# Kernel tuning notes

Hardware: AMD Instinct MI355X
Metric: run time of the kernel (lower is better)

## Reference

```python
import jax, jax.numpy as jnp
import numpy as np


def setup_inputs() -> dict:
    key = jax.random.key(0)
    n_samples, n_points, dims = 16, 2048, 64
    h = jax.random.normal(key, (n_samples, n_points, dims), dtype=jnp.float32)
    return {"h": h, "K": 16}


def reference(h, K):
    """Pairwise squared distance + K nearest neighbors -> edge list.

    h : (n_samples, n_points, dims)
    Returns (knn_dist, dst, src):
      knn_dist : (n_samples, n_points, K) squared distances to the K nearest points
      dst, src : (n_samples*n_points*K,) int32 globally-offset edge endpoints
    """
    n_samples, n_points, _ = h.shape
    # d[b, i, j] = ||h[b,i]||^2 + ||h[b,j]||^2 - 2 <h[b,i], h[b,j]>
    x2s = jnp.sum(h * h, axis=-1, keepdims=True)          # (s, n, 1)
    d = x2s + jnp.swapaxes(x2s, -1, -2) - 2.0 * jnp.einsum('bnd,bmd->bnm', h, h)
    # smallest-K == top-K of negated distances (matches torch.topk largest=False order)
    neg_vals, k_indices = jax.lax.top_k(-d, K)            # (s, n, K)
    knn_dist = -neg_vals
    # edge list with per-sample node-id offsets (matches the torch flattening)
    src = jnp.broadcast_to(jnp.arange(n_points, dtype=k_indices.dtype)[None, :, None],
                           k_indices.shape)
    offset = (jnp.arange(n_samples, dtype=k_indices.dtype) * n_points)[:, None, None]
    dst = (k_indices + offset).reshape(-1)
    src = (src + offset).reshape(-1)
    return knn_dist, dst, src
```

## Files before the change

### kernel.cpp

```cpp
#include <hip/hip_runtime.h>
#include <hip/hip_fp16.h>
#include <cfloat>


typedef _Float16 half8 __attribute__((ext_vector_type(8)));
typedef _Float16 half4 __attribute__((ext_vector_type(4)));
typedef float    f32x4 __attribute__((ext_vector_type(4)));

constexpr int NS = 16, NP = 2048, ND = 64, KK = 16;
constexpr int NWV = 4;
constexpr int NT  = NWV * 64;
constexpr int RB  = 64;
constexpr int ITN = RB / 16;
constexpr int JW  = NP / NWV;
constexpr int NJT = JW / 16;
constexpr int MS  = 17;
constexpr int RCAP = 176;
constexpr int RSTR = RCAP + 1;
constexpr float MARGIN = 1.0f;

__global__ __launch_bounds__(256)
void prep_kernel(const float* __restrict__ h, float* __restrict__ x2,
                 _Float16* __restrict__ hh)
{
    const int b = blockIdx.x;
    const int t = threadIdx.x;
    const size_t base = (size_t)b * 16 * ND;

    float4 v = *(const float4*)(h + base + (size_t)t * 4);
    half4 p;
    p[0] = (_Float16)v.x; p[1] = (_Float16)v.y;
    p[2] = (_Float16)v.z; p[3] = (_Float16)v.w;
    *(half4*)(hh + base + (size_t)t * 4) = p;

    if (t < 16) {
        const int g = b * 16 + t;
        const float4* row = (const float4*)(h + (size_t)g * ND);
        const int ph = g & 15;
        float a0 = 0.f, a1 = 0.f, a2 = 0.f, a3 = 0.f;
        #pragma unroll
        for (int k = 0; k < 16; ++k) {
            float4 u = row[(k + ph) & 15];
            a0 = fmaf(u.x, u.x, a0); a1 = fmaf(u.y, u.y, a1);
            a2 = fmaf(u.z, u.z, a2); a3 = fmaf(u.w, u.w, a3);
        }
        x2[g] = (a0 + a1) + (a2 + a3);
    }
}

__device__ __forceinline__ bool lexlt(float a, int ja, float b, int jb)
{
    return (a < b) || (a == b && ja < jb);
}
__device__ __forceinline__ void insert16x(float (&d)[KK], int (&ix)[KK],
                                          float v, int j)
{
    #pragma unroll
    for (int p = KK - 1; p > 0; --p) {
        bool sh = lexlt(v, j, d[p - 1], ix[p - 1]);
        bool he = lexlt(v, j, d[p], ix[p]);
        float nd = sh ? d[p - 1] : (he ? v : d[p]);
        int   ni = sh ? ix[p - 1] : (he ? j : ix[p]);
        d[p] = nd; ix[p] = ni;
    }
    if (lexlt(v, j, d[0], ix[0])) { d[0] = v; ix[0] = j; }
}

__device__ __forceinline__ void bitonic4(float &a1, float &a2, float &a3,
                                         float &a4, int mask)
{
    float b1 = __shfl_xor(a1, mask), b2 = __shfl_xor(a2, mask);
    float b3 = __shfl_xor(a3, mask), b4 = __shfl_xor(a4, mask);
    float m1 = fminf(a1, b4), m2 = fminf(a2, b3);
    float m3 = fminf(a3, b2), m4 = fminf(a4, b1);
    float u1 = fminf(m1, m3), u3 = fmaxf(m1, m3);
    float u2 = fminf(m2, m4), u4 = fmaxf(m2, m4);
    a1 = fminf(u1, u2); a2 = fmaxf(u1, u2);
    a3 = fminf(u3, u4); a4 = fmaxf(u3, u4);
}

__global__ __launch_bounds__(NT, 2)
void knn_mfma(const float* __restrict__ h, const _Float16* __restrict__ hh,
              const float* __restrict__ x2g, float* __restrict__ out)
{
    __shared__ __align__(16) float smem[18112];
    float* ldsx2  = smem;
    float* mw     = smem + 2048;
    float* ldsthr = smem + 2304;
    int*   rcnt   = (int*)(smem + 2368);
    int*   ring   = (int*)(smem + 2432);
    float* md     = smem + 13760;
    int*   mi     = (int*)(smem + 15936);

    const int t   = threadIdx.x;
    const int ln  = t & 63;
    const int qd  = ln >> 4;
    const int cl  = ln & 15;
    const int q   = t >> 6;
    const int bid = blockIdx.x;
    const int xcd = bid & 7;
    const int kb  = bid >> 3;
    const int s   = xcd + ((kb & 1) << 3);
    const int rb  = kb >> 1;
    const int rowbase = rb * RB;
    const float*    __restrict__ hs  = h  + (size_t)s * NP * ND;
    const _Float16* __restrict__ hhs = hh + (size_t)s * NP * ND;

    ((float4*)ldsx2)[t]       = ((const float4*)(x2g + s * NP))[t];
    ((float4*)ldsx2)[t + 256] = ((const float4*)(x2g + s * NP))[t + 256];
    if (t < RB) rcnt[t] = 0;

    half8 ifr[ITN][2];
    #pragma unroll
    for (int it = 0; it < ITN; ++it) {
        const _Float16* ap = hhs + (size_t)(rowbase + it * 16 + cl) * ND + qd * 8;
        ifr[it][0] = *(const half8*)(ap);
        ifr[it][1] = *(const half8*)(ap + 32);
    }
    __syncthreads();

    const int jbase = q * JW;
    const _Float16* __restrict__ jrow0 = hhs + (size_t)(jbase + cl) * ND + qd * 8;

    float t1[ITN], t2[ITN], t3[ITN], t4[ITN];
    #pragma unroll
    for (int it = 0; it < ITN; ++it)
        { t1[it] = FLT_MAX; t2[it] = FLT_MAX; t3[it] = FLT_MAX; t4[it] = FLT_MAX; }

    #pragma unroll 2
    for (int jt = 0; jt < NJT; ++jt) {
        const _Float16* bp = jrow0 + (size_t)jt * (16 * ND);
        half8 jlo = *(const half8*)(bp);
        half8 jhi = *(const half8*)(bp + 32);
        f32x4 xq = *(const f32x4*)(ldsx2 + jbase + jt * 16 + qd * 4);

        #pragma unroll
        for (int it = 0; it < ITN; ++it) {
            f32x4 acc;
            acc = __builtin_amdgcn_mfma_f32_16x16x32_f16(
                      jlo, ifr[it][0], (f32x4){0.f, 0.f, 0.f, 0.f}, 0, 0, 0);
            acc = __builtin_amdgcn_mfma_f32_16x16x32_f16(
                      jhi, ifr[it][1], acc, 0, 0, 0);
            #pragma unroll
            for (int r = 0; r < 4; ++r) {
                float v  = fmaf(-2.f, acc[r], xq[r]);
                float n1 = fminf(t1[it], v);
                float n2 = __builtin_amdgcn_fmed3f(t1[it], t2[it], v);
                float n3 = __builtin_amdgcn_fmed3f(t2[it], t3[it], v);
                float n4 = __builtin_amdgcn_fmed3f(t3[it], t4[it], v);
                t1[it] = n1; t2[it] = n2; t3[it] = n3; t4[it] = n4;
            }
        }
    }

    #pragma unroll
    for (int it = 0; it < ITN; ++it) {
        bitonic4(t1[it], t2[it], t3[it], t4[it], 16);
        bitonic4(t1[it], t2[it], t3[it], t4[it], 32);
    }
    if (qd == 0) {
        #pragma unroll
        for (int it = 0; it < ITN; ++it)
            mw[q * RB + it * 16 + cl] = t4[it];
    }
    __syncthreads();
    if (q == 0) {
        float m0 = mw[ln],            m1 = mw[RB + ln];
        float m2 = mw[2 * RB + ln],   m3 = mw[3 * RB + ln];
        ldsthr[ln] = fmaxf(fmaxf(m0, m1), fmaxf(m2, m3)) + MARGIN;
    }
    __syncthreads();

    float thrv[ITN];
    #pragma unroll
    for (int it = 0; it < ITN; ++it) thrv[it] = ldsthr[it * 16 + cl];

    #pragma unroll 2
    for (int jt = 0; jt < NJT; ++jt) {
        const _Float16* bp = jrow0 + (size_t)jt * (16 * ND);
        half8 jlo = *(const half8*)(bp);
        half8 jhi = *(const half8*)(bp + 32);
        f32x4 xq = *(const f32x4*)(ldsx2 + jbase + jt * 16 + qd * 4);
        const int j0 = jbase + jt * 16;

        #pragma unroll
        for (int it = 0; it < ITN; ++it) {
            f32x4 acc;
            acc = __builtin_amdgcn_mfma_f32_16x16x32_f16(
                      jlo, ifr[it][0], (f32x4){0.f, 0.f, 0.f, 0.f}, 0, 0, 0);
            acc = __builtin_amdgcn_mfma_f32_16x16x32_f16(
                      jhi, ifr[it][1], acc, 0, 0, 0);
            #pragma unroll
            for (int r = 0; r < 4; ++r) {
                float d2 = fmaf(-2.f, acc[r], xq[r]);
                if (d2 < thrv[it]) {
                    int rw = it * 16 + cl;
                    int slot = atomicAdd(&rcnt[rw], 1);
                    if (slot < RCAP) ring[rw * RSTR + slot] = j0 + qd * 4 + r;
                }
            }
        }
    }
    __syncthreads();

    const int row   = ln;
    const int myrow = rowbase + row;
    float4 A[16];
    {
        const float4* ra = (const float4*)(hs + (size_t)myrow * ND);
        #pragma unroll
        for (int k = 0; k < 16; ++k) A[k] = ra[k];
    }
    float x2i;
    {
        float a0 = 0.f, a1 = 0.f, a2 = 0.f, a3 = 0.f;
        #pragma unroll
        for (int k = 0; k < 16; ++k) {
            a0 = fmaf(A[k].x, A[k].x, a0); a1 = fmaf(A[k].y, A[k].y, a1);
            a2 = fmaf(A[k].z, A[k].z, a2); a3 = fmaf(A[k].w, A[k].w, a3);
        }
        x2i = (a0 + a1) + (a2 + a3);
    }
    float dist[KK]; int idx[KK];
    #pragma unroll
    for (int k = 0; k < KK; ++k) { dist[k] = FLT_MAX; idx[k] = 0; }

    const int rawc = rcnt[row];
    if (rawc <= RCAP) {
        #pragma unroll 1
        for (int k = q; k < rawc; k += NWV) {
            int j = ring[row * RSTR + k];
            const float4* cv = (const float4*)(hs + (size_t)j * ND);
            float a0 = 0.f, a1 = 0.f, a2 = 0.f, a3 = 0.f;
            #pragma unroll
            for (int kk = 0; kk < 16; ++kk) {
                float4 c = cv[kk];
                a0 = fmaf(A[kk].x, c.x, a0); a1 = fmaf(A[kk].y, c.y, a1);
                a2 = fmaf(A[kk].z, c.z, a2); a3 = fmaf(A[kk].w, c.w, a3);
            }
            float dotv = (a0 + a1) + (a2 + a3);
            float d2 = fmaf(-2.0f, dotv, x2i + ldsx2[j]);
            if (lexlt(d2, j, dist[KK - 1], idx[KK - 1]))
                insert16x(dist, idx, d2, j);
        }
    } else {
        #pragma unroll 1
        for (int j = q; j < NP; j += NWV) {
            const float4* cv = (const float4*)(hs + (size_t)j * ND);
            float a0 = 0.f, a1 = 0.f, a2 = 0.f, a3 = 0.f;
            #pragma unroll
            for (int kk = 0; kk < 16; ++kk) {
                float4 c = cv[kk];
                a0 = fmaf(A[kk].x, c.x, a0); a1 = fmaf(A[kk].y, c.y, a1);
                a2 = fmaf(A[kk].z, c.z, a2); a3 = fmaf(A[kk].w, c.w, a3);
            }
            float dotv = (a0 + a1) + (a2 + a3);
            float d2 = fmaf(-2.0f, dotv, x2i + ldsx2[j]);
            if (lexlt(d2, j, dist[KK - 1], idx[KK - 1]))
                insert16x(dist, idx, d2, j);
        }
    }

    __syncthreads();
    #pragma unroll 1
    for (int lvl = 0; lvl < 2; ++lvl) {
        const int step = 1 << lvl;
        const int m    = (step << 1) - 1;
        const bool pub = ((q & m) == step);
        const int reg  = q >> (lvl + 1);
        if (pub) {
            #pragma unroll
            for (int k = 0; k < KK; ++k) {
                md[(reg * RB + row) * MS + k] = dist[k];
                mi[(reg * RB + row) * MS + k] = idx[k];
            }
        }
        __syncthreads();
        if ((q & m) == 0) {
            #pragma unroll 1
            for (int k = 0; k < KK; ++k) {
                float v  = md[(reg * RB + row) * MS + k];
                int   jv = mi[(reg * RB + row) * MS + k];
                bool need = lexlt(v, jv, dist[KK - 1], idx[KK - 1]);
                if (!__any(need)) break;
                if (need) insert16x(dist, idx, v, jv);
            }
        }
        __syncthreads();
    }

    if (q == 0) {
        const int off = s * NP;
        const size_t rg = (size_t)off + myrow;
        float* o0 = out + rg * KK;
        float* o1 = out + (size_t)NS * NP * KK + rg * KK;
        float* o2 = out + (size_t)2 * NS * NP * KK + rg * KK;
        #pragma unroll
        for (int k = 0; k < KK; ++k) o0[k] = dist[k];
        #pragma unroll
        for (int k = 0; k < KK; ++k) o1[k] = (float)(idx[k] + off);
        #pragma unroll
        for (int k = 0; k < KK; ++k) o2[k] = (float)(off + myrow);
    }
}

extern "C" void kernel_launch(void* const* d_in, const int* in_sizes, int n_in,
                              void* d_out, int out_size, void* d_ws, size_t ws_size,
                              hipStream_t stream)
{
    const float* h = (const float*)d_in[0];
    float* out = (float*)d_out;
    float*    x2 = (float*)d_ws;
    _Float16* hh = (_Float16*)(x2 + NS * NP);

    hipLaunchKernelGGL(prep_kernel, dim3(NS * NP / 16), dim3(256), 0, stream,
                       h, x2, hh);
    hipLaunchKernelGGL(knn_mfma, dim3(NS * (NP / RB)), dim3(NT), 0, stream,
                       h, hh, x2, out);
}
```

Baseline: 178.2 us.

## Double block rows and waves, track top-2 per lane for KNN threshold

Each block now handles 128 query rows with 8 waves instead of 64 rows with 4. Every j-tile fp16 fragment loaded for the MFMA distance passes is therefore reused across twice as many rows. The pre-pass threshold now keeps only the two smallest distances per lane, since 8 waves × 2 still guarantees at least 16 candidates, which cuts the med3 work and register pressure. The candidate ring capacity is reduced, and the merge buffers are aliased onto the ring to fit LDS. The risks are more fallback full scans when a row overflows the smaller ring, and higher per-block register use that can limit occupancy.

```diff
diff --git a/kernel.cpp b/kernel.cpp
--- a/kernel.cpp
+++ b/kernel.cpp
@@ -8,14 +8,14 @@
 typedef float    f32x4 __attribute__((ext_vector_type(4)));
 
 constexpr int NS = 16, NP = 2048, ND = 64, KK = 16;
-constexpr int NWV = 4;
+constexpr int NWV = 8;
 constexpr int NT  = NWV * 64;
-constexpr int RB  = 64;
+constexpr int RB  = 128;
 constexpr int ITN = RB / 16;
 constexpr int JW  = NP / NWV;
 constexpr int NJT = JW / 16;
 constexpr int MS  = 17;
-constexpr int RCAP = 176;
+constexpr int RCAP = 127;
 constexpr int RSTR = RCAP + 1;
 constexpr float MARGIN = 1.0f;
 
@@ -66,31 +66,18 @@
     if (lexlt(v, j, d[0], ix[0])) { d[0] = v; ix[0] = j; }
 }
 
-__device__ __forceinline__ void bitonic4(float &a1, float &a2, float &a3,
-                                         float &a4, int mask)
-{
-    float b1 = __shfl_xor(a1, mask), b2 = __shfl_xor(a2, mask);
-    float b3 = __shfl_xor(a3, mask), b4 = __shfl_xor(a4, mask);
-    float m1 = fminf(a1, b4), m2 = fminf(a2, b3);
-    float m3 = fminf(a3, b2), m4 = fminf(a4, b1);
-    float u1 = fminf(m1, m3), u3 = fmaxf(m1, m3);
-    float u2 = fminf(m2, m4), u4 = fmaxf(m2, m4);
-    a1 = fminf(u1, u2); a2 = fmaxf(u1, u2);
-    a3 = fminf(u3, u4); a4 = fmaxf(u3, u4);
-}
-
 __global__ __launch_bounds__(NT, 2)
 void knn_mfma(const float* __restrict__ h, const _Float16* __restrict__ hh,
               const float* __restrict__ x2g, float* __restrict__ out)
 {
-    __shared__ __align__(16) float smem[18112];
+    __shared__ __align__(16) float smem[19712];
     float* ldsx2  = smem;
     float* mw     = smem + 2048;
-    float* ldsthr = smem + 2304;
-    int*   rcnt   = (int*)(smem + 2368);
-    int*   ring   = (int*)(smem + 2432);
-    float* md     = smem + 13760;
-    int*   mi     = (int*)(smem + 15936);
+    float* ldsthr = smem + 3072;
+    int*   rcnt   = (int*)(smem + 3200);
+    int*   ring   = (int*)(smem + 3328);
+    float* md     = (float*)ring;
+    int*   mi     = ring + 4352;
 
     const int t   = threadIdx.x;
     const int ln  = t & 63;
@@ -106,8 +93,7 @@
     const float*    __restrict__ hs  = h  + (size_t)s * NP * ND;
     const _Float16* __restrict__ hhs = hh + (size_t)s * NP * ND;
 
-    ((float4*)ldsx2)[t]       = ((const float4*)(x2g + s * NP))[t];
-    ((float4*)ldsx2)[t + 256] = ((const float4*)(x2g + s * NP))[t + 256];
+    ((float4*)ldsx2)[t] = ((const float4*)(x2g + s * NP))[t];
     if (t < RB) rcnt[t] = 0;
 
     half8 ifr[ITN][2];
@@ -122,10 +108,9 @@
     const int jbase = q * JW;
     const _Float16* __restrict__ jrow0 = hhs + (size_t)(jbase + cl) * ND + qd * 8;
 
-    float t1[ITN], t2[ITN], t3[ITN], t4[ITN];
-    #pragma unroll
-    for (int it = 0; it < ITN; ++it)
-        { t1[it] = FLT_MAX; t2[it] = FLT_MAX; t3[it] = FLT_MAX; t4[it] = FLT_MAX; }
+    float t1[ITN], t2[ITN];
+    #pragma unroll
+    for (int it = 0; it < ITN; ++it) { t1[it] = FLT_MAX; t2[it] = FLT_MAX; }
 
     #pragma unroll 2
     for (int jt = 0; jt < NJT; ++jt) {
@@ -146,28 +131,37 @@
                 float v  = fmaf(-2.f, acc[r], xq[r]);
                 float n1 = fminf(t1[it], v);
                 float n2 = __builtin_amdgcn_fmed3f(t1[it], t2[it], v);
-                float n3 = __builtin_amdgcn_fmed3f(t2[it], t3[it], v);
-                float n4 = __builtin_amdgcn_fmed3f(t3[it], t4[it], v);
-                t1[it] = n1; t2[it] = n2; t3[it] = n3; t4[it] = n4;
+                t1[it] = n1; t2[it] = n2;
             }
         }
     }
 
     #pragma unroll
     for (int it = 0; it < ITN; ++it) {
-        bitonic4(t1[it], t2[it], t3[it], t4[it], 16);
-        bitonic4(t1[it], t2[it], t3[it], t4[it], 32);
+        #pragma unroll
+        for (int lvl = 0; lvl < 2; ++lvl) {
+            const int mask = 16 << lvl;
+            float b1 = __shfl_xor(t1[it], mask), b2 = __shfl_xor(t2[it], mask);
+            float m1 = fminf(t1[it], b2), m2 = fminf(t2[it], b1);
+            t1[it] = fminf(m1, m2);
+            t2[it] = fmaxf(m1, m2);
+        }
     }
     if (qd == 0) {
         #pragma unroll
         for (int it = 0; it < ITN; ++it)
-            mw[q * RB + it * 16 + cl] = t4[it];
+            mw[q * RB + it * 16 + cl] = t2[it];
     }
     __syncthreads();
     if (q == 0) {
-        float m0 = mw[ln],            m1 = mw[RB + ln];
-        float m2 = mw[2 * RB + ln],   m3 = mw[3 * RB + ln];
-        ldsthr[ln] = fmaxf(fmaxf(m0, m1), fmaxf(m2, m3)) + MARGIN;
+        #pragma unroll
+        for (int hf = 0; hf < 2; ++hf) {
+            const int rw = ln + hf * 64;
+            float m = mw[rw];
+            #pragma unroll
+            for (int w = 1; w < NWV; ++w) m = fmaxf(m, mw[w * RB + rw]);
+            ldsthr[rw] = m + MARGIN;
+        }
     }
     __syncthreads();
 
@@ -203,7 +197,8 @@
     }
     __syncthreads();
 
-    const int row   = ln;
+    const int row   = (q & 1) * 64 + ln;
+    const int w     = q >> 1;
     const int myrow = rowbase + row;
     float4 A[16];
     {
@@ -228,7 +223,7 @@
     const int rawc = rcnt[row];
     if (rawc <= RCAP) {
         #pragma unroll 1
-        for (int k = q; k < rawc; k += NWV) {
+        for (int k = w; k < rawc; k += 4) {
             int j = ring[row * RSTR + k];
             const float4* cv = (const float4*)(hs + (size_t)j * ND);
             float a0 = 0.f, a1 = 0.f, a2 = 0.f, a3 = 0.f;
@@ -245,7 +240,7 @@
         }
     } else {
         #pragma unroll 1
-        for (int j = q; j < NP; j += NWV) {
+        for (int j = w; j < NP; j += 4) {
             const float4* cv = (const float4*)(hs + (size_t)j * ND);
             float a0 = 0.f, a1 = 0.f, a2 = 0.f, a3 = 0.f;
             #pragma unroll
@@ -266,8 +261,8 @@
     for (int lvl = 0; lvl < 2; ++lvl) {
         const int step = 1 << lvl;
         const int m    = (step << 1) - 1;
-        const bool pub = ((q & m) == step);
-        const int reg  = q >> (lvl + 1);
+        const bool pub = ((w & m) == step);
+        const int reg  = w >> (lvl + 1);
         if (pub) {
             #pragma unroll
             for (int k = 0; k < KK; ++k) {
@@ -276,7 +271,7 @@
             }
         }
         __syncthreads();
-        if ((q & m) == 0) {
+        if ((w & m) == 0) {
             #pragma unroll 1
             for (int k = 0; k < KK; ++k) {
                 float v  = md[(reg * RB + row) * MS + k];
@@ -289,7 +284,7 @@
         __syncthreads();
     }
 
-    if (q == 0) {
+    if (q < 2) {
         const int off = s * NP;
         const size_t rg = (size_t)off + myrow;
         float* o0 = out + rg * KK;
```

Measured after the change: 638.2 us. 3.58x slower.
